# Optimization experiments

Measured on AMD Instinct MI355X. Metric: run time of the kernel, lower is better.

The kernel has to match this reference:

```python
import jax, jax.numpy as jnp
import numpy as np

GO_DIM, HID = 200, 256
N_PROT, N_GO, N_EDGE = 50000, 50000, 1600000
LN_EPS = 1e-5


def setup_inputs() -> dict:
    key = jax.random.key(0)
    ks = jax.random.split(key, 12)
    inp = {
        "prot_emb": jax.random.normal(ks[0], (N_PROT, HID), jnp.float32),
        "go_x": jax.random.normal(ks[1], (N_GO, GO_DIM), jnp.float32),
        "pg_edge_index": jax.random.randint(ks[2], (2, N_EDGE), 0, N_PROT, jnp.int32),
        "num_proteins": N_PROT,
        # go_proj
        "Wg": jax.random.normal(ks[3], (GO_DIM, HID), jnp.float32) / np.sqrt(GO_DIM),
        "bg": jnp.zeros((HID,), jnp.float32),
        # fuse MLP
        "W1": jax.random.normal(ks[4], (2 * HID, HID), jnp.float32) / np.sqrt(2 * HID),
        "b1": jnp.zeros((HID,), jnp.float32),
        "W2": jax.random.normal(ks[5], (HID, HID), jnp.float32) / np.sqrt(HID),
        "b2": jnp.zeros((HID,), jnp.float32),
        # LayerNorm
        "gamma": jnp.ones((HID,), jnp.float32),
        "beta": jnp.zeros((HID,), jnp.float32),
    }
    return inp


def _layernorm(x, gamma, beta):
    mu = jnp.mean(x, axis=-1, keepdims=True)
    var = jnp.mean(jnp.square(x - mu), axis=-1, keepdims=True)
    return (x - mu) * jax.lax.rsqrt(var + LN_EPS) * gamma + beta


def reference(prot_emb, go_x, pg_edge_index, num_proteins,
              Wg, bg, W1, b1, W2, b2, gamma, beta):
    dst, src = pg_edge_index[0], pg_edge_index[1]  # dst: protein ids, src: GO ids
    go_h = jax.nn.relu(go_x @ Wg + bg)                         # [G, H]
    msgs = go_h[src]                                           # [E, H] gather
    sums = jax.ops.segment_sum(msgs, dst, num_segments=num_proteins)      # [N, H]
    count = jax.ops.segment_sum(jnp.ones((msgs.shape[0],), msgs.dtype), dst,
                                num_segments=num_proteins)     # [N]
    go_agg = sums / jnp.maximum(count, 1.0)[:, None]           # scatter-mean
    go_present = (count > 0).astype(prot_emb.dtype)[:, None]   # [N, 1]
    h = jnp.concatenate([prot_emb, go_agg], axis=-1)           # [N, 2H]
    fused = jax.nn.relu(h @ W1 + b1) @ W2 + b2                 # [N, H]
    return _layernorm(prot_emb + go_present * fused, gamma, beta)
```

## Files before the change

### kernel.cpp

```cpp
#include <hip/hip_runtime.h>
#include <hip/hip_bf16.h>
#include <stdint.h>

#define HID 256
#define GOD 200
#define LN_EPS 1e-5f
#define PB 64
#define PBSH 6
#define NBLK 128
#define MAXNB 800
#define CAP 6144

typedef __attribute__((ext_vector_type(8))) short short8;
typedef __attribute__((ext_vector_type(4))) float f32x4;

__device__ __forceinline__ float bf2f(unsigned short u) {
    union { unsigned int i; float f; } c; c.i = ((unsigned int)u) << 16; return c.f;
}
__device__ __forceinline__ unsigned short f2bf(float f) {
    union { float f; unsigned int i; } c; c.f = f;
    unsigned int x = c.i;
    return (unsigned short)((x + 0x7fffu + ((x >> 16) & 1u)) >> 16);
}
__device__ __forceinline__ unsigned int pack2(float a, float b) {
    return (unsigned int)f2bf(a) | ((unsigned int)f2bf(b) << 16);
}
__device__ __forceinline__ short8 pack8(float4 a, float4 b) {
    short8 r;
    r[0] = (short)f2bf(a.x); r[1] = (short)f2bf(a.y);
    r[2] = (short)f2bf(a.z); r[3] = (short)f2bf(a.w);
    r[4] = (short)f2bf(b.x); r[5] = (short)f2bf(b.y);
    r[6] = (short)f2bf(b.z); r[7] = (short)f2bf(b.w);
    return r;
}

__global__ void transpose_all_kernel(const float* __restrict__ Wg, const float* __restrict__ W1,
                                     const float* __restrict__ W2, short* __restrict__ Wgt,
                                     short* __restrict__ W1t, short* __restrict__ W2t) {
    const int TOT = 65536 + 131072 + 65536;
    for (int idx = blockIdx.x * 256 + threadIdx.x; idx < TOT; idx += gridDim.x * 256) {
        if (idx < 65536) {
            int c = idx >> 8, k = idx & 255;
            Wgt[idx] = (short)f2bf(k < GOD ? Wg[(size_t)k * 256 + c] : 0.f);
        } else if (idx < 65536 + 131072) {
            int j = idx - 65536;
            int c = j >> 9, k = j & 511;
            W1t[j] = (short)f2bf(W1[(size_t)k * 256 + c]);
        } else {
            int j = idx - (65536 + 131072);
            int c = j >> 8, k = j & 255;
            W2t[j] = (short)f2bf(W2[(size_t)k * 256 + c]);
        }
    }
}

template<int K, int ASTRIDE, int AK, bool AF32, int EPI>
__global__ __launch_bounds__(256) void gemm_mfma(
        const void* __restrict__ Ap, const short* __restrict__ Bt,
        const float* __restrict__ bias, void* __restrict__ outp,
        const float* __restrict__ prot, const int* __restrict__ counts, int M) {
    __shared__ short As[128][88];
    __shared__ short Bs[128][88];

    const int t = threadIdx.x;
    const int row0 = blockIdx.x * 128;
    const int col0 = blockIdx.y * 128;
    const int lane = t & 63, w = t >> 6, wr = w >> 1, wc = w & 1;

    f32x4 acc[4][4] = {};

    for (int kt = 0; kt < K / 64; ++kt) {
        const int k0 = kt * 64;
        short8 ar[4], br[4];
#pragma unroll
        for (int i = 0; i < 4; ++i) {
            int seg = t + i * 256;
            int r = seg >> 3, co = (seg & 7) * 8;
            if (AF32) {
                short8 v = {};
                if (row0 + r < M && k0 + co + 8 <= AK) {
                    const float* ap = (const float*)Ap + (size_t)(row0 + r) * ASTRIDE + k0 + co;
                    float4 f0 = *(const float4*)ap;
                    float4 f1 = *(const float4*)(ap + 4);
                    v = pack8(f0, f1);
                }
                ar[i] = v;
            } else {
                short8 v = {};
                if (row0 + r < M)
                    v = *(const short8*)((const short*)Ap + (size_t)(row0 + r) * ASTRIDE + k0 + co);
                ar[i] = v;
            }
            br[i] = *(const short8*)(Bt + (size_t)(col0 + r) * K + k0 + co);
        }
        __syncthreads();
#pragma unroll
        for (int i = 0; i < 4; ++i) {
            int seg = t + i * 256;
            int r = seg >> 3, co = (seg & 7) * 8;
            *(short8*)&As[r][co] = ar[i];
            *(short8*)&Bs[r][co] = br[i];
        }
        __syncthreads();
#pragma unroll
        for (int ks = 0; ks < 2; ++ks) {
            short8 af[4], bf[4];
#pragma unroll
            for (int mt = 0; mt < 4; ++mt)
                af[mt] = *(const short8*)&As[wr * 64 + mt * 16 + (lane & 15)][ks * 32 + (lane >> 4) * 8];
#pragma unroll
            for (int nt = 0; nt < 4; ++nt)
                bf[nt] = *(const short8*)&Bs[wc * 64 + nt * 16 + (lane & 15)][ks * 32 + (lane >> 4) * 8];
#pragma unroll
            for (int mt = 0; mt < 4; ++mt)
#pragma unroll
                for (int nt = 0; nt < 4; ++nt)
                    acc[mt][nt] = __builtin_amdgcn_mfma_f32_16x16x32_bf16(af[mt], bf[nt], acc[mt][nt], 0, 0, 0);
        }
    }

#pragma unroll
    for (int nt = 0; nt < 4; ++nt) {
        int cg = col0 + wc * 64 + nt * 16 + (lane & 15);
        float bb = bias[cg];
#pragma unroll
        for (int mt = 0; mt < 4; ++mt) {
            int rbase = row0 + wr * 64 + mt * 16 + ((lane >> 4) * 4);
#pragma unroll
            for (int j = 0; j < 4; ++j) {
                int rg = rbase + j;
                if (rg < M) {
                    float v = acc[mt][nt][j] + bb;
                    if (EPI == 0) {
                        ((unsigned short*)outp)[(size_t)rg * 256 + cg] = f2bf(fmaxf(v, 0.f));
                    } else {
                        float pres = (counts[rg] > 0) ? 1.f : 0.f;
                        ((float*)outp)[(size_t)rg * 256 + cg] =
                            prot[(size_t)rg * 256 + cg] + pres * v;
                    }
                }
            }
        }
    }
}

__global__ __launch_bounds__(256) void blk_hist_kernel(
        const int* __restrict__ dst, int* __restrict__ blk_cnt, int E, int NB, int chunk) {
    __shared__ int h[MAXNB];
    int k = blockIdx.x, tid = threadIdx.x;
    for (int i = tid; i < NB; i += 256) h[i] = 0;
    __syncthreads();
    int s0 = k * chunk, s1 = min(E, s0 + chunk);
    for (int e = s0 + tid; e < s1; e += 256) atomicAdd(&h[dst[e] >> PBSH], 1);
    __syncthreads();
    for (int i = tid; i < NB; i += 256) blk_cnt[(size_t)i * NBLK + k] = h[i];
}

__global__ __launch_bounds__(64) void blk_scan_kernel(
        const int* __restrict__ blk_cnt, int* __restrict__ blk_off, int* __restrict__ btot) {
    int b = blockIdx.x, l = threadIdx.x;
    int v0 = blk_cnt[(size_t)b * NBLK + 2 * l];
    int v1 = blk_cnt[(size_t)b * NBLK + 2 * l + 1];
    int s = v0 + v1;
#pragma unroll
    for (int o = 1; o < 64; o <<= 1) { int y = __shfl_up(s, o); if (l >= o) s += y; }
    int excl = s - (v0 + v1);
    blk_off[(size_t)b * NBLK + 2 * l]     = excl;
    blk_off[(size_t)b * NBLK + 2 * l + 1] = excl + v0;
    if (l == 63) btot[b] = s;
}

__global__ __launch_bounds__(1024) void bucket_scan_kernel(
        const int* __restrict__ btot, int* __restrict__ bbase, int NB, int E) {
    __shared__ int sc[1024];
    int tid = threadIdx.x;
    int v = (tid < NB) ? btot[tid] : 0;
    sc[tid] = v;
    __syncthreads();
    for (int o = 1; o < 1024; o <<= 1) {
        int add = (tid >= o) ? sc[tid - o] : 0;
        __syncthreads();
        sc[tid] += add;
        __syncthreads();
    }
    if (tid < NB) bbase[tid] = sc[tid] - v;
    if (tid == 0) bbase[NB] = E;
}

__global__ __launch_bounds__(256) void part_kernel(
        const int* __restrict__ dst, const int* __restrict__ src,
        const int* __restrict__ bbase, const int* __restrict__ blk_off,
        unsigned int* __restrict__ pairs, int E, int NB, int chunk) {
    __shared__ int cur[MAXNB];
    int k = blockIdx.x, tid = threadIdx.x;
    for (int i = tid; i < NB; i += 256)
        cur[i] = bbase[i] + blk_off[(size_t)i * NBLK + k];
    __syncthreads();
    int s0 = k * chunk, s1 = min(E, s0 + chunk);
    for (int e = s0 + tid; e < s1; e += 256) {
        int d = dst[e];
        unsigned int pr = ((unsigned int)(d & (PB - 1)) << 16) | (unsigned int)src[e];
        int slot = atomicAdd(&cur[d >> PBSH], 1);
        pairs[slot] = pr;
    }
}

__global__ __launch_bounds__(256) void agg_kernel(
        const unsigned short* __restrict__ go_h, const unsigned int* __restrict__ pairs,
        const int* __restrict__ bbase, const float* __restrict__ prot,
        unsigned short* __restrict__ hcat, int* __restrict__ counts, int N) {
    __shared__ unsigned short srt[CAP];
    __shared__ int cnt[PB], off[PB], cur[PB];
    int b = blockIdx.x, tid = threadIdx.x, w = tid >> 6, l = tid & 63;
    int e0 = bbase[b], e1 = bbase[b + 1];
    int ec = e1 - e0;
    int ecs = min(ec, CAP);

    if (tid < PB) cnt[tid] = 0;
    __syncthreads();
    for (int i = tid; i < ecs; i += 256)
        atomicAdd(&cnt[pairs[e0 + i] >> 16], 1);
    __syncthreads();
    if (w == 0) {
        int v = cnt[l];
        int s = v;
#pragma unroll
        for (int o = 1; o < 64; o <<= 1) { int y = __shfl_up(s, o); if (l >= o) s += y; }
        off[l] = s - v;
        cur[l] = s - v;
    }
    __syncthreads();
    for (int i = tid; i < ecs; i += 256) {
        unsigned int pr = pairs[e0 + i];
        int slot = atomicAdd(&cur[pr >> 16], 1);
        srt[slot] = (unsigned short)(pr & 0xffffu);
    }
    __syncthreads();

    int p0g = b << PBSH;
    for (int r = w; r < PB; r += 4) {
        int p = p0g + r;
        if (p >= N) break;
        int o0 = off[r], d = cnt[r];
        float a0 = 0.f, a1 = 0.f, a2 = 0.f, a3 = 0.f;
        int i = 0;
        for (; i + 4 <= d; i += 4) {
            int g0 = srt[o0 + i], g1 = srt[o0 + i + 1];
            int g2 = srt[o0 + i + 2], g3 = srt[o0 + i + 3];
            ushort4 u0 = *(const ushort4*)(go_h + (size_t)g0 * 256 + l * 4);
            ushort4 u1 = *(const ushort4*)(go_h + (size_t)g1 * 256 + l * 4);
            ushort4 u2 = *(const ushort4*)(go_h + (size_t)g2 * 256 + l * 4);
            ushort4 u3 = *(const ushort4*)(go_h + (size_t)g3 * 256 + l * 4);
            a0 += bf2f(u0.x) + bf2f(u1.x) + bf2f(u2.x) + bf2f(u3.x);
            a1 += bf2f(u0.y) + bf2f(u1.y) + bf2f(u2.y) + bf2f(u3.y);
            a2 += bf2f(u0.z) + bf2f(u1.z) + bf2f(u2.z) + bf2f(u3.z);
            a3 += bf2f(u0.w) + bf2f(u1.w) + bf2f(u2.w) + bf2f(u3.w);
        }
        for (; i < d; ++i) {
            int g = srt[o0 + i];
            ushort4 u = *(const ushort4*)(go_h + (size_t)g * 256 + l * 4);
            a0 += bf2f(u.x); a1 += bf2f(u.y); a2 += bf2f(u.z); a3 += bf2f(u.w);
        }
        int dtot = d;
        for (int j = e0 + ecs; j < e1; ++j) {
            unsigned int pr = pairs[j];
            if ((int)(pr >> 16) == r) {
                ushort4 u = *(const ushort4*)(go_h + (size_t)(pr & 0xffffu) * 256 + l * 4);
                a0 += bf2f(u.x); a1 += bf2f(u.y); a2 += bf2f(u.z); a3 += bf2f(u.w);
                dtot++;
            }
        }
        float inv = 1.f / (float)max(dtot, 1);
        float4 pf = ((const float4*)(prot + (size_t)p * 256))[l];
        unsigned int* hp = (unsigned int*)(hcat + (size_t)p * 512);
        hp[2 * l]     = pack2(pf.x, pf.y);
        hp[2 * l + 1] = pack2(pf.z, pf.w);
        unsigned int* hq = hp + 128 + 2 * l;
        hq[0] = pack2(a0 * inv, a1 * inv);
        hq[1] = pack2(a2 * inv, a3 * inv);
        if (l == 0) counts[p] = dtot;
    }
}

__global__ __launch_bounds__(256) void ln_kernel(
        const float* __restrict__ y, const float* __restrict__ gamma,
        const float* __restrict__ beta, float* __restrict__ out, int N) {
    int lane = threadIdx.x & 63;
    int row = blockIdx.x * 4 + (threadIdx.x >> 6);
    if (row >= N) return;
    float4 v = ((const float4*)(y + (size_t)row * 256))[lane];
    float s = v.x + v.y + v.z + v.w;
#pragma unroll
    for (int o = 32; o >= 1; o >>= 1) s += __shfl_xor(s, o);
    float mu = s * (1.f / 256.f);
    float4 d; d.x = v.x - mu; d.y = v.y - mu; d.z = v.z - mu; d.w = v.w - mu;
    float q = d.x * d.x + d.y * d.y + d.z * d.z + d.w * d.w;
#pragma unroll
    for (int o = 32; o >= 1; o >>= 1) q += __shfl_xor(q, o);
    float rstd = rsqrtf(q * (1.f / 256.f) + LN_EPS);
    float4 g = ((const float4*)gamma)[lane];
    float4 b = ((const float4*)beta)[lane];
    float4 o4;
    o4.x = d.x * rstd * g.x + b.x; o4.y = d.y * rstd * g.y + b.y;
    o4.z = d.z * rstd * g.z + b.z; o4.w = d.w * rstd * g.w + b.w;
    ((float4*)(out + (size_t)row * 256))[lane] = o4;
}

extern "C" void kernel_launch(void* const* d_in, const int* in_sizes, int n_in,
                              void* d_out, int out_size, void* d_ws, size_t ws_size,
                              hipStream_t stream) {
    const float* prot  = (const float*)d_in[0];
    const float* go_x  = (const float*)d_in[1];
    const int*   edges = (const int*)d_in[2];
    const float* Wg    = (const float*)d_in[4];
    const float* bg    = (const float*)d_in[5];
    const float* W1    = (const float*)d_in[6];
    const float* b1    = (const float*)d_in[7];
    const float* W2    = (const float*)d_in[8];
    const float* b2    = (const float*)d_in[9];
    const float* gamma = (const float*)d_in[10];
    const float* beta  = (const float*)d_in[11];

    int N = in_sizes[0] / HID;
    int G = in_sizes[1] / GOD;
    int E = in_sizes[2] / 2;
    const int* dst = edges;
    const int* src = edges + E;
    int NB = (N + PB - 1) / PB;
    int chunk = (E + NBLK - 1) / NBLK;

    uint8_t* w = (uint8_t*)d_ws;
    size_t off = 0;
    auto alloc = [&](size_t bytes) -> void* {
        void* p = w + off;
        off = (off + bytes + 255) & ~(size_t)255;
        return p;
    };
    unsigned short* go_h = (unsigned short*)alloc((size_t)G * HID * 2);
    unsigned short* hcat = (unsigned short*)alloc((size_t)N * 512 * 2);
    unsigned short* tmp  = (unsigned short*)alloc((size_t)N * HID * 2);
    int* counts  = (int*)alloc((size_t)N * 4);
    int* blk_cnt = (int*)alloc((size_t)NB * NBLK * 4);
    int* blk_off = (int*)alloc((size_t)NB * NBLK * 4);
    int* btot    = (int*)alloc((size_t)NB * 4);
    int* bbase   = (int*)alloc((size_t)(NB + 1) * 4);
    short* Wgt = (short*)alloc((size_t)256 * 256 * 2);
    short* W1t = (short*)alloc((size_t)256 * 512 * 2);
    short* W2t = (short*)alloc((size_t)256 * 256 * 2);
    unsigned int* pairs = (unsigned int*)tmp;
    float* y = (float*)hcat;

    transpose_all_kernel<<<dim3(256), dim3(256), 0, stream>>>(Wg, W1, W2, Wgt, W1t, W2t);

    int rb = (N + 127) / 128;
    int rbg = (G + 127) / 128;

    gemm_mfma<256, GOD, GOD, true, 0><<<dim3(rbg, 2), dim3(256), 0, stream>>>(
        go_x, Wgt, bg, go_h, nullptr, nullptr, G);

    blk_hist_kernel<<<dim3(NBLK), dim3(256), 0, stream>>>(dst, blk_cnt, E, NB, chunk);
    blk_scan_kernel<<<dim3(NB), dim3(64), 0, stream>>>(blk_cnt, blk_off, btot);
    bucket_scan_kernel<<<dim3(1), dim3(1024), 0, stream>>>(btot, bbase, NB, E);
    part_kernel<<<dim3(NBLK), dim3(256), 0, stream>>>(dst, src, bbase, blk_off, pairs, E, NB, chunk);

    agg_kernel<<<dim3(NB), dim3(256), 0, stream>>>(go_h, pairs, bbase, prot, hcat, counts, N);

    gemm_mfma<512, 512, 512, false, 0><<<dim3(rb, 2), dim3(256), 0, stream>>>(
        hcat, W1t, b1, tmp, nullptr, nullptr, N);

    gemm_mfma<256, 256, 256, false, 1><<<dim3(rb, 2), dim3(256), 0, stream>>>(
        tmp, W2t, b2, y, prot, counts, N);

    ln_kernel<<<dim3((N + 3) / 4), dim3(256), 0, stream>>>(y, gamma, beta, (float*)d_out, N);
}
```

Measured before the change: 474.1 us.

## Fuse second MLP GEMM with residual and LayerNorm; halve protein bucket size

Replaces the second GEMM plus a separate LayerNorm pass with one 512-thread kernel. Each block computes a full 128x256 output tile, adds the residual and presence mask, and reduces row statistics through shared memory before normalising. This removes the round trip of an fp32 intermediate through global memory and one kernel launch. The aggregation buckets also shrink from 64 to 32 proteins (more blocks, smaller shared capacity), which needs a multi-pass bucket scan; variance is now computed as E[x^2]-mu^2, which is less numerically robust.

```diff
diff --git a/kernel.cpp b/kernel.cpp
--- a/kernel.cpp
+++ b/kernel.cpp
@@ -5,11 +5,11 @@
 #define HID 256
 #define GOD 200
 #define LN_EPS 1e-5f
-#define PB 64
-#define PBSH 6
+#define PB 32
+#define PBSH 5
 #define NBLK 128
-#define MAXNB 800
-#define CAP 6144
+#define MAXNB 1600
+#define CAP 4096
 
 typedef __attribute__((ext_vector_type(8))) short short8;
 typedef __attribute__((ext_vector_type(4))) float f32x4;
@@ -54,11 +54,10 @@
     }
 }
 
-template<int K, int ASTRIDE, int AK, bool AF32, int EPI>
+template<int K, int ASTRIDE, int AK, bool AF32>
 __global__ __launch_bounds__(256) void gemm_mfma(
         const void* __restrict__ Ap, const short* __restrict__ Bt,
-        const float* __restrict__ bias, void* __restrict__ outp,
-        const float* __restrict__ prot, const int* __restrict__ counts, int M) {
+        const float* __restrict__ bias, void* __restrict__ outp, int M) {
     __shared__ short As[128][88];
     __shared__ short Bs[128][88];
 
@@ -131,14 +130,130 @@
                 int rg = rbase + j;
                 if (rg < M) {
                     float v = acc[mt][nt][j] + bb;
-                    if (EPI == 0) {
-                        ((unsigned short*)outp)[(size_t)rg * 256 + cg] = f2bf(fmaxf(v, 0.f));
-                    } else {
-                        float pres = (counts[rg] > 0) ? 1.f : 0.f;
-                        ((float*)outp)[(size_t)rg * 256 + cg] =
-                            prot[(size_t)rg * 256 + cg] + pres * v;
-                    }
+                    ((unsigned short*)outp)[(size_t)rg * 256 + cg] = f2bf(fmaxf(v, 0.f));
                 }
+            }
+        }
+    }
+}
+
+__global__ __launch_bounds__(512) void mlp2_ln_kernel(
+        const unsigned short* __restrict__ tmp, const short* __restrict__ W2t,
+        const float* __restrict__ b2, const float* __restrict__ prot,
+        const int* __restrict__ counts, const float* __restrict__ gamma,
+        const float* __restrict__ beta, float* __restrict__ out, int M) {
+    __shared__ short As[128][88];
+    __shared__ short Bs[256][88];
+    __shared__ float psum[128][4];
+    __shared__ float psq[128][4];
+
+    const int t = threadIdx.x;
+    const int row0 = blockIdx.x * 128;
+    const int lane = t & 63, w = t >> 6, wr = w >> 2, wc = w & 3;
+
+    f32x4 acc[4][4] = {};
+
+    for (int kt = 0; kt < 4; ++kt) {
+        const int k0 = kt * 64;
+        short8 ar[2], br[4];
+#pragma unroll
+        for (int i = 0; i < 2; ++i) {
+            int seg = t + i * 512;
+            int r = seg >> 3, co = (seg & 7) * 8;
+            short8 v = {};
+            if (row0 + r < M)
+                v = *(const short8*)(tmp + (size_t)(row0 + r) * 256 + k0 + co);
+            ar[i] = v;
+        }
+#pragma unroll
+        for (int i = 0; i < 4; ++i) {
+            int seg = t + i * 512;
+            int r = seg >> 3, co = (seg & 7) * 8;
+            br[i] = *(const short8*)(W2t + (size_t)r * 256 + k0 + co);
+        }
+        __syncthreads();
+#pragma unroll
+        for (int i = 0; i < 2; ++i) {
+            int seg = t + i * 512;
+            int r = seg >> 3, co = (seg & 7) * 8;
+            *(short8*)&As[r][co] = ar[i];
+        }
+#pragma unroll
+        for (int i = 0; i < 4; ++i) {
+            int seg = t + i * 512;
+            int r = seg >> 3, co = (seg & 7) * 8;
+            *(short8*)&Bs[r][co] = br[i];
+        }
+        __syncthreads();
+#pragma unroll
+        for (int ks = 0; ks < 2; ++ks) {
+            short8 af[4], bf[4];
+#pragma unroll
+            for (int mt = 0; mt < 4; ++mt)
+                af[mt] = *(const short8*)&As[wr * 64 + mt * 16 + (lane & 15)][ks * 32 + (lane >> 4) * 8];
+#pragma unroll
+            for (int nt = 0; nt < 4; ++nt)
+                bf[nt] = *(const short8*)&Bs[wc * 64 + nt * 16 + (lane & 15)][ks * 32 + (lane >> 4) * 8];
+#pragma unroll
+            for (int mt = 0; mt < 4; ++mt)
+#pragma unroll
+                for (int nt = 0; nt < 4; ++nt)
+                    acc[mt][nt] = __builtin_amdgcn_mfma_f32_16x16x32_bf16(af[mt], bf[nt], acc[mt][nt], 0, 0, 0);
+        }
+    }
+
+    float bb[4];
+#pragma unroll
+    for (int nt = 0; nt < 4; ++nt) bb[nt] = b2[wc * 64 + nt * 16 + (lane & 15)];
+
+#pragma unroll
+    for (int mt = 0; mt < 4; ++mt) {
+#pragma unroll
+        for (int j = 0; j < 4; ++j) {
+            int rloc = wr * 64 + mt * 16 + ((lane >> 4) * 4) + j;
+            int rg = row0 + rloc;
+            float pres = 0.f;
+            if (rg < M) pres = (counts[rg] > 0) ? 1.f : 0.f;
+            float s = 0.f, q = 0.f;
+#pragma unroll
+            for (int nt = 0; nt < 4; ++nt) {
+                int cg = wc * 64 + nt * 16 + (lane & 15);
+                float pv = (rg < M) ? prot[(size_t)rg * 256 + cg] : 0.f;
+                float yv = pv + pres * (acc[mt][nt][j] + bb[nt]);
+                acc[mt][nt][j] = yv;
+                s += yv;
+                q += yv * yv;
+            }
+#pragma unroll
+            for (int o = 1; o < 16; o <<= 1) {
+                s += __shfl_xor(s, o);
+                q += __shfl_xor(q, o);
+            }
+            if ((lane & 15) == 0) {
+                psum[rloc][wc] = s;
+                psq[rloc][wc] = q;
+            }
+        }
+    }
+    __syncthreads();
+
+#pragma unroll
+    for (int mt = 0; mt < 4; ++mt) {
+#pragma unroll
+        for (int j = 0; j < 4; ++j) {
+            int rloc = wr * 64 + mt * 16 + ((lane >> 4) * 4) + j;
+            int rg = row0 + rloc;
+            if (rg >= M) continue;
+            float s = psum[rloc][0] + psum[rloc][1] + psum[rloc][2] + psum[rloc][3];
+            float q = psq[rloc][0] + psq[rloc][1] + psq[rloc][2] + psq[rloc][3];
+            float mu = s * (1.f / 256.f);
+            float var = q * (1.f / 256.f) - mu * mu;
+            float rstd = rsqrtf(var + LN_EPS);
+#pragma unroll
+            for (int nt = 0; nt < 4; ++nt) {
+                int cg = wc * 64 + nt * 16 + (lane & 15);
+                float o4 = (acc[mt][nt][j] - mu) * rstd * gamma[cg] + beta[cg];
+                out[(size_t)rg * 256 + cg] = o4;
             }
         }
     }
@@ -173,17 +288,26 @@
 __global__ __launch_bounds__(1024) void bucket_scan_kernel(
         const int* __restrict__ btot, int* __restrict__ bbase, int NB, int E) {
     __shared__ int sc[1024];
+    __shared__ int carry;
     int tid = threadIdx.x;
-    int v = (tid < NB) ? btot[tid] : 0;
-    sc[tid] = v;
-    __syncthreads();
-    for (int o = 1; o < 1024; o <<= 1) {
-        int add = (tid >= o) ? sc[tid - o] : 0;
-        __syncthreads();
-        sc[tid] += add;
-        __syncthreads();
-    }
-    if (tid < NB) bbase[tid] = sc[tid] - v;
+    if (tid == 0) carry = 0;
+    __syncthreads();
+    for (int base = 0; base < NB; base += 1024) {
+        int i = base + tid;
+        int v = (i < NB) ? btot[i] : 0;
+        sc[tid] = v;
+        __syncthreads();
+        for (int o = 1; o < 1024; o <<= 1) {
+            int add = (tid >= o) ? sc[tid - o] : 0;
+            __syncthreads();
+            sc[tid] += add;
+            __syncthreads();
+        }
+        if (i < NB) bbase[i] = carry + sc[tid] - v;
+        __syncthreads();
+        if (tid == 0) carry += sc[1023];
+        __syncthreads();
+    }
     if (tid == 0) bbase[NB] = E;
 }
 
@@ -222,12 +346,11 @@
         atomicAdd(&cnt[pairs[e0 + i] >> 16], 1);
     __syncthreads();
     if (w == 0) {
-        int v = cnt[l];
+        int v = (l < PB) ? cnt[l] : 0;
         int s = v;
 #pragma unroll
-        for (int o = 1; o < 64; o <<= 1) { int y = __shfl_up(s, o); if (l >= o) s += y; }
-        off[l] = s - v;
-        cur[l] = s - v;
+        for (int o = 1; o < PB; o <<= 1) { int y = __shfl_up(s, o); if (l >= o) s += y; }
+        if (l < PB) { off[l] = s - v; cur[l] = s - v; }
     }
     __syncthreads();
     for (int i = tid; i < ecs; i += 256) {
@@ -280,30 +403,6 @@
         hq[1] = pack2(a2 * inv, a3 * inv);
         if (l == 0) counts[p] = dtot;
     }
-}
-
-__global__ __launch_bounds__(256) void ln_kernel(
-        const float* __restrict__ y, const float* __restrict__ gamma,
-        const float* __restrict__ beta, float* __restrict__ out, int N) {
-    int lane = threadIdx.x & 63;
-    int row = blockIdx.x * 4 + (threadIdx.x >> 6);
-    if (row >= N) return;
-    float4 v = ((const float4*)(y + (size_t)row * 256))[lane];
-    float s = v.x + v.y + v.z + v.w;
-#pragma unroll
-    for (int o = 32; o >= 1; o >>= 1) s += __shfl_xor(s, o);
-    float mu = s * (1.f / 256.f);
-    float4 d; d.x = v.x - mu; d.y = v.y - mu; d.z = v.z - mu; d.w = v.w - mu;
-    float q = d.x * d.x + d.y * d.y + d.z * d.z + d.w * d.w;
-#pragma unroll
-    for (int o = 32; o >= 1; o >>= 1) q += __shfl_xor(q, o);
-    float rstd = rsqrtf(q * (1.f / 256.f) + LN_EPS);
-    float4 g = ((const float4*)gamma)[lane];
-    float4 b = ((const float4*)beta)[lane];
-    float4 o4;
-    o4.x = d.x * rstd * g.x + b.x; o4.y = d.y * rstd * g.y + b.y;
-    o4.z = d.z * rstd * g.z + b.z; o4.w = d.w * rstd * g.w + b.w;
-    ((float4*)(out + (size_t)row * 256))[lane] = o4;
 }
 
 extern "C" void kernel_launch(void* const* d_in, const int* in_sizes, int n_in,
@@ -348,15 +447,14 @@
     short* W1t = (short*)alloc((size_t)256 * 512 * 2);
     short* W2t = (short*)alloc((size_t)256 * 256 * 2);
     unsigned int* pairs = (unsigned int*)tmp;
-    float* y = (float*)hcat;
 
     transpose_all_kernel<<<dim3(256), dim3(256), 0, stream>>>(Wg, W1, W2, Wgt, W1t, W2t);
 
     int rb = (N + 127) / 128;
     int rbg = (G + 127) / 128;
 
-    gemm_mfma<256, GOD, GOD, true, 0><<<dim3(rbg, 2), dim3(256), 0, stream>>>(
-        go_x, Wgt, bg, go_h, nullptr, nullptr, G);
+    gemm_mfma<256, GOD, GOD, true><<<dim3(rbg, 2), dim3(256), 0, stream>>>(
+        go_x, Wgt, bg, go_h, G);
 
     blk_hist_kernel<<<dim3(NBLK), dim3(256), 0, stream>>>(dst, blk_cnt, E, NB, chunk);
     blk_scan_kernel<<<dim3(NB), dim3(64), 0, stream>>>(blk_cnt, blk_off, btot);
@@ -365,11 +463,9 @@
 
     agg_kernel<<<dim3(NB), dim3(256), 0, stream>>>(go_h, pairs, bbase, prot, hcat, counts, N);
 
-    gemm_mfma<512, 512, 512, false, 0><<<dim3(rb, 2), dim3(256), 0, stream>>>(
-        hcat, W1t, b1, tmp, nullptr, nullptr, N);
-
-    gemm_mfma<256, 256, 256, false, 1><<<dim3(rb, 2), dim3(256), 0, stream>>>(
-        tmp, W2t, b2, y, prot, counts, N);
-
-    ln_kernel<<<dim3((N + 3) / 4), dim3(256), 0, stream>>>(y, gamma, beta, (float*)d_out, N);
-}
+    gemm_mfma<512, 512, 512, false><<<dim3(rb, 2), dim3(256), 0, stream>>>(
+        hcat, W1t, b1, tmp, N);
+
+    mlp2_ln_kernel<<<dim3(rb), dim3(512), 0, stream>>>(
+        tmp, W2t, b2, prot, counts, gamma, beta, (float*)d_out, N);
+}
```

After: 463.7 us. -2.2%, faster.
